# Kernel optimization log

Measured on AMD Instinct MI355X. Metric: run time of the kernel, lower is better.

Reference implementation:

```python
import jax, jax.numpy as jnp
import numpy as np

N = 1024
DIM = 128
HEADS = 8
DK = DIM // HEADS
EDIM = 16
EPS = 1e-5
NEG = -10000.0


def _lin(k, din, dout):
    return jax.random.normal(k, (din, dout), jnp.float32) * (1.0 / np.sqrt(din))


def setup_inputs() -> dict:
    key = jax.random.key(0)
    ks = jax.random.split(key, 10)
    mask = jax.random.randint(ks[2], (N, N), 0, 2).astype(bool)
    mask = mask | jnp.eye(N, dtype=bool)  # self-loops always valid
    return {
        "x": jax.random.normal(ks[0], (N, DIM), jnp.float32),
        "edge_feat": jax.random.normal(ks[1], (N, N, EDIM), jnp.float32),
        "mask": mask,
        "Wq": _lin(ks[3], DIM, DIM), "bq": jnp.zeros((DIM,), jnp.float32),
        "Wk": _lin(ks[4], DIM, DIM), "bk": jnp.zeros((DIM,), jnp.float32),
        "Wv": _lin(ks[5], DIM, DIM), "bv": jnp.zeros((DIM,), jnp.float32),
        "Wae": _lin(ks[6], EDIM, HEADS), "bae": jnp.zeros((HEADS,), jnp.float32),
        "Wve": _lin(ks[7], EDIM, DIM), "bve": jnp.zeros((DIM,), jnp.float32),
        "Wo": _lin(ks[8], DIM, DIM), "bo": jnp.zeros((DIM,), jnp.float32),
        "gamma": jnp.ones((DIM,), jnp.float32),
        "beta": jnp.zeros((DIM,), jnp.float32),
    }


def reference(x, edge_feat, mask, Wq, bq, Wk, bk, Wv, bv, Wae, bae, Wve, bve, Wo, bo, gamma, beta):
    n, dim = x.shape
    heads = bae.shape[0]
    dk = dim // heads
    # pre-LayerNorm
    mu = jnp.mean(x, axis=-1, keepdims=True)
    var = jnp.mean(jnp.square(x - mu), axis=-1, keepdims=True)
    h = (x - mu) * jax.lax.rsqrt(var + EPS) * gamma + beta
    q = (h @ Wq + bq).reshape(n, heads, dk)
    k = (h @ Wk + bk).reshape(n, heads, dk)
    v = (h @ Wv + bv).reshape(n, heads, dk)
    # attention logits with per-edge additive bias: (n, m, heads)
    att = jnp.einsum('nhd,mhd->nmh', q, k) / np.sqrt(dk).astype(np.float32)
    att = att + edge_feat @ Wae + bae
    att = jnp.where(mask[..., None], att, NEG)
    alpha = jax.nn.softmax(att, axis=1)  # softmax over source nodes m
    # edge-conditioned values: msg_{nm} = v_m + U(e_{nm})
    edge_val = (edge_feat @ Wve + bve).reshape(n, n, heads, dk)
    out = jnp.einsum('nmh,mhd->nhd', alpha, v) + jnp.einsum('nmh,nmhd->nhd', alpha, edge_val)
    out = out.reshape(n, dim) @ Wo + bo
    return x + out
```

## Files before the change

### kernel.cpp

```cpp
#include <hip/hip_runtime.h>
#include <hip/hip_bf16.h>

#define NNODE 1024
#define DIM 128
#define HEADS 8
#define DK 16
#define EDIM 16
#define BN 8
#define MR 32
#define EF_ROW 20
#define EF_NSTR 644
#define LOG2E 1.44269504f

__global__ __launch_bounds__(384)
void ln_qkv_kernel(const float* __restrict__ x,
                   const float* __restrict__ Wq, const float* __restrict__ bq,
                   const float* __restrict__ Wk, const float* __restrict__ bk,
                   const float* __restrict__ Wv, const float* __restrict__ bv,
                   const float* __restrict__ gamma, const float* __restrict__ beta,
                   float* __restrict__ qg, float* __restrict__ kg, float* __restrict__ vg) {
    const int n = blockIdx.x;
    const int t = threadIdx.x;
    __shared__ float hrow[DIM];
    __shared__ float part[4];

    float xv = 0.f;
    if (t < 128) {
        xv = x[n * DIM + t];
        float v = xv;
        #pragma unroll
        for (int off = 32; off >= 1; off >>= 1) v += __shfl_xor(v, off);
        if ((t & 63) == 0) part[t >> 6] = v;
    }
    __syncthreads();
    const float mu = (part[0] + part[1]) * (1.0f / DIM);
    const float dx = xv - mu;
    if (t < 128) {
        float v = dx * dx;
        #pragma unroll
        for (int off = 32; off >= 1; off >>= 1) v += __shfl_xor(v, off);
        if ((t & 63) == 0) part[2 + (t >> 6)] = v;
    }
    __syncthreads();
    if (t < 128) {
        const float var = (part[2] + part[3]) * (1.0f / DIM);
        hrow[t] = dx * rsqrtf(var + 1e-5f) * gamma[t] + beta[t];
    }
    __syncthreads();

    const int which = t >> 7;
    const int col = t & 127;
    const float* W = (which == 0) ? Wq : (which == 1) ? Wk : Wv;
    const float* b = (which == 0) ? bq : (which == 1) ? bk : bv;
    float* o       = (which == 0) ? qg : (which == 1) ? kg : vg;
    float acc = b[col];
    #pragma unroll 16
    for (int i = 0; i < DIM; ++i) acc = fmaf(hrow[i], W[i * DIM + col], acc);
    o[n * DIM + col] = acc;
}

__global__ __launch_bounds__(256, 2)
void attn_kernel(const float* __restrict__ qg, const float* __restrict__ kg,
                 const float* __restrict__ vg, const float* __restrict__ ef,
                 const int* __restrict__ mask,
                 const float* __restrict__ Wae, const float* __restrict__ bae,
                 float* __restrict__ acc) {
    const int t = threadIdx.x;
    const int s  = t >> 5;
    const int np = (t >> 3) & 3;
    const int h  = t & 7;
    const int wid = t >> 6, lane = t & 63;
    const int bx = blockIdx.x;
    const int n0 = (bx >> 5) * BN;
    const int mb = (bx & 31) * MR;

    __shared__ float ef_lds[BN * EF_NSTR];
    __shared__ int   mk_lds[BN * 34];

    #pragma unroll
    for (int r = 0; r < 4; ++r) {
        const int idx = t + 256 * r;
        const int nn = idx >> 7;
        const int mm = (idx >> 2) & 31;
        const int q4 = idx & 3;
        const float4 ev = *(const float4*)(ef + ((size_t)(n0 + nn) * NNODE + mb + mm) * EDIM + q4 * 4);
        *(float4*)&ef_lds[nn * EF_NSTR + mm * EF_ROW + q4 * 4] = ev;
    }
    {
        const int nn = t >> 5, mm = t & 31;
        mk_lds[nn * 34 + mm] = mask[(size_t)(n0 + nn) * NNODE + (mb + mm)];
    }
    float qreg[2][DK];
    #pragma unroll
    for (int hf = 0; hf < 2; ++hf) {
        const float* qp = qg + (size_t)(n0 + np + 4 * hf) * DIM + h * DK;
        #pragma unroll
        for (int d4 = 0; d4 < 4; ++d4) {
            const float4 qv = *(const float4*)(qp + d4 * 4);
            qreg[hf][d4 * 4 + 0] = qv.x; qreg[hf][d4 * 4 + 1] = qv.y;
            qreg[hf][d4 * 4 + 2] = qv.z; qreg[hf][d4 * 4 + 3] = qv.w;
        }
    }
    float waec[EDIM];
    #pragma unroll
    for (int e = 0; e < EDIM; ++e) waec[e] = Wae[e * HEADS + h] * LOG2E;
    const float baeh = bae[h] * LOG2E;

    float sl[2] = {0.f, 0.f};
    float accv[2][DK], accT[2][EDIM];
    #pragma unroll
    for (int hf = 0; hf < 2; ++hf) {
        #pragma unroll
        for (int d = 0; d < DK; ++d) accv[hf][d] = 0.f;
        #pragma unroll
        for (int e = 0; e < EDIM; ++e) accT[hf][e] = 0.f;
    }

    __syncthreads();

    #pragma unroll 1
    for (int j = 0; j < 4; ++j) {
        const int m = j * 8 + s;
        const size_t gm = (size_t)(mb + m);
        float kk[DK], vv[DK];
        const float* kp = kg + gm * DIM + h * DK;
        const float* vp = vg + gm * DIM + h * DK;
        #pragma unroll
        for (int d4 = 0; d4 < 4; ++d4) {
            const float4 k4 = *(const float4*)(kp + d4 * 4);
            kk[d4 * 4 + 0] = k4.x; kk[d4 * 4 + 1] = k4.y;
            kk[d4 * 4 + 2] = k4.z; kk[d4 * 4 + 3] = k4.w;
            const float4 v4 = *(const float4*)(vp + d4 * 4);
            vv[d4 * 4 + 0] = v4.x; vv[d4 * 4 + 1] = v4.y;
            vv[d4 * 4 + 2] = v4.z; vv[d4 * 4 + 3] = v4.w;
        }
        #pragma unroll
        for (int hf = 0; hf < 2; ++hf) {
            const int n = np + 4 * hf;
            const float* ep = &ef_lds[n * EF_NSTR + m * EF_ROW];
            float efv[EDIM];
            #pragma unroll
            for (int e4 = 0; e4 < 4; ++e4) {
                const float4 ev = *(const float4*)(ep + e4 * 4);
                efv[e4 * 4 + 0] = ev.x; efv[e4 * 4 + 1] = ev.y;
                efv[e4 * 4 + 2] = ev.z; efv[e4 * 4 + 3] = ev.w;
            }
            float bias = baeh, dot = 0.f;
            #pragma unroll
            for (int e = 0; e < EDIM; ++e) bias = fmaf(efv[e], waec[e], bias);
            #pragma unroll
            for (int d = 0; d < DK; ++d) dot = fmaf(qreg[hf][d], kk[d], dot);
            const float lg = fmaf(dot, 0.25f * LOG2E, bias);
            const float p = mk_lds[n * 34 + m] ? __builtin_amdgcn_exp2f(lg) : 0.f;
            sl[hf] += p;
            #pragma unroll
            for (int d = 0; d < DK; ++d) accv[hf][d] = fmaf(p, vv[d], accv[hf][d]);
            #pragma unroll
            for (int e = 0; e < EDIM; ++e) accT[hf][e] = fmaf(p, efv[e], accT[hf][e]);
        }
    }

    #pragma unroll
    for (int hf = 0; hf < 2; ++hf) {
        sl[hf] += __shfl_xor(sl[hf], 32);
        #pragma unroll
        for (int d = 0; d < DK; ++d) accv[hf][d] += __shfl_xor(accv[hf][d], 32);
        #pragma unroll
        for (int e = 0; e < EDIM; ++e) accT[hf][e] += __shfl_xor(accT[hf][e], 32);
    }
    __syncthreads();
    float* redA = ef_lds;
    float* redB = ef_lds + BN * HEADS * 33;
    if (lane < 32 && wid < 2) {
        float* base = (wid == 0) ? redA : redB;
        #pragma unroll
        for (int hf = 0; hf < 2; ++hf) {
            float* rp = base + ((np + 4 * hf) * 8 + h) * 33;
            rp[0] = sl[hf];
            #pragma unroll
            for (int d = 0; d < DK; ++d) rp[1 + d] = accv[hf][d];
            #pragma unroll
            for (int e = 0; e < EDIM; ++e) rp[17 + e] = accT[hf][e];
        }
    }
    __syncthreads();
    if (lane < 32 && wid >= 2) {
        float* base = (wid == 2) ? redA : redB;
        #pragma unroll
        for (int hf = 0; hf < 2; ++hf) {
            float* rp = base + ((np + 4 * hf) * 8 + h) * 33;
            rp[0] += sl[hf];
            #pragma unroll
            for (int d = 0; d < DK; ++d) rp[1 + d] += accv[hf][d];
            #pragma unroll
            for (int e = 0; e < EDIM; ++e) rp[17 + e] += accT[hf][e];
        }
    }
    __syncthreads();
    for (int u = t; u < BN * HEADS * 33; u += 256)
        atomicAdd(&acc[(size_t)n0 * HEADS * 33 + u], redA[u] + redB[u]);
}

__global__ __launch_bounds__(128)
void final_kernel(const float* __restrict__ acc,
                  const float* __restrict__ Wve, const float* __restrict__ bve,
                  const float* __restrict__ x,
                  const float* __restrict__ Wo, const float* __restrict__ bo,
                  float* __restrict__ out) {
    const int n = blockIdx.x, t = threadIdx.x;
    __shared__ float ab[HEADS * 33];
    __shared__ float orow[DIM];
    for (int u = t; u < HEADS * 33; u += 128) ab[u] = acc[(size_t)n * HEADS * 33 + u];
    __syncthreads();
    const int col = t, hh = col >> 4, dd = col & 15;
    const float slv = ab[hh * 33];
    float acc2 = 0.f;
    #pragma unroll
    for (int e = 0; e < EDIM; ++e) acc2 = fmaf(ab[hh * 33 + 17 + e], Wve[e * DIM + col], acc2);
    orow[col] = (ab[hh * 33 + 1 + dd] + acc2) / slv + bve[col];
    __syncthreads();
    float o = bo[col] + x[(size_t)n * DIM + col];
    #pragma unroll 16
    for (int i = 0; i < DIM; ++i) o = fmaf(orow[i], Wo[i * DIM + col], o);
    out[(size_t)n * DIM + col] = o;
}

extern "C" void kernel_launch(void* const* d_in, const int* in_sizes, int n_in,
                              void* d_out, int out_size, void* d_ws, size_t ws_size,
                              hipStream_t stream) {
    const float* x     = (const float*)d_in[0];
    const float* ef    = (const float*)d_in[1];
    const int*   mask  = (const int*)d_in[2];
    const float* Wq    = (const float*)d_in[3];
    const float* bq    = (const float*)d_in[4];
    const float* Wk    = (const float*)d_in[5];
    const float* bk    = (const float*)d_in[6];
    const float* Wv    = (const float*)d_in[7];
    const float* bv    = (const float*)d_in[8];
    const float* Wae   = (const float*)d_in[9];
    const float* bae   = (const float*)d_in[10];
    const float* Wve   = (const float*)d_in[11];
    const float* bve   = (const float*)d_in[12];
    const float* Wo    = (const float*)d_in[13];
    const float* bo    = (const float*)d_in[14];
    const float* gamma = (const float*)d_in[15];
    const float* beta  = (const float*)d_in[16];

    float* ws = (float*)d_ws;
    float* accb = ws;
    float* qg   = ws + 270336;
    float* kg   = qg + (size_t)NNODE * DIM;
    float* vg   = kg + (size_t)NNODE * DIM;

    hipMemsetAsync(accb, 0, (size_t)NNODE * HEADS * 33 * sizeof(float), stream);
    ln_qkv_kernel<<<NNODE, 384, 0, stream>>>(x, Wq, bq, Wk, bk, Wv, bv, gamma, beta, qg, kg, vg);
    attn_kernel<<<(NNODE / BN) * 32, 256, 0, stream>>>(qg, kg, vg, ef, mask, Wae, bae, accb);
    final_kernel<<<NNODE, 128, 0, stream>>>(accb, Wve, bve, x, Wo, bo, (float*)d_out);
}
```

Measured before the change: 200.4 us.

## Read edge features and mask directly from global, halve m-split block count

Drops the shared-memory staging of edge features and mask, so each thread loads its edge-feature row and mask value straight from global memory inside the loop. The source-node range per block doubles (16 splits instead of 32), so each block loops over 8 iterations with unroll 2 instead of 4, and fewer partial results go through the atomic accumulation. This removes the LDS copy and a barrier but gives up coalesced staging: each thread now reads 64 contiguous bytes per edge with a wider stride between lanes, and there are fewer blocks to hide latency.

```diff
diff --git a/kernel.cpp b/kernel.cpp
--- a/kernel.cpp
+++ b/kernel.cpp
@@ -7,9 +7,9 @@
 #define DK 16
 #define EDIM 16
 #define BN 8
-#define MR 32
-#define EF_ROW 20
-#define EF_NSTR 644
+#define MSPLIT 16
+#define MRANGE (NNODE / MSPLIT)
+#define NJ (MRANGE / 8)
 #define LOG2E 1.44269504f
 
 __global__ __launch_bounds__(384)
@@ -71,25 +71,11 @@
     const int h  = t & 7;
     const int wid = t >> 6, lane = t & 63;
     const int bx = blockIdx.x;
-    const int n0 = (bx >> 5) * BN;
-    const int mb = (bx & 31) * MR;
-
-    __shared__ float ef_lds[BN * EF_NSTR];
-    __shared__ int   mk_lds[BN * 34];
-
-    #pragma unroll
-    for (int r = 0; r < 4; ++r) {
-        const int idx = t + 256 * r;
-        const int nn = idx >> 7;
-        const int mm = (idx >> 2) & 31;
-        const int q4 = idx & 3;
-        const float4 ev = *(const float4*)(ef + ((size_t)(n0 + nn) * NNODE + mb + mm) * EDIM + q4 * 4);
-        *(float4*)&ef_lds[nn * EF_NSTR + mm * EF_ROW + q4 * 4] = ev;
-    }
-    {
-        const int nn = t >> 5, mm = t & 31;
-        mk_lds[nn * 34 + mm] = mask[(size_t)(n0 + nn) * NNODE + (mb + mm)];
-    }
+    const int n0 = (bx >> 4) * BN;
+    const int mb = (bx & 15) * MRANGE;
+
+    __shared__ float red2[2 * BN * HEADS * 33];
+
     float qreg[2][DK];
     #pragma unroll
     for (int hf = 0; hf < 2; ++hf) {
@@ -116,15 +102,12 @@
         for (int e = 0; e < EDIM; ++e) accT[hf][e] = 0.f;
     }
 
-    __syncthreads();
-
-    #pragma unroll 1
-    for (int j = 0; j < 4; ++j) {
-        const int m = j * 8 + s;
-        const size_t gm = (size_t)(mb + m);
+    #pragma unroll 2
+    for (int j = 0; j < NJ; ++j) {
+        const int gm = mb + j * 8 + s;
         float kk[DK], vv[DK];
-        const float* kp = kg + gm * DIM + h * DK;
-        const float* vp = vg + gm * DIM + h * DK;
+        const float* kp = kg + (size_t)gm * DIM + h * DK;
+        const float* vp = vg + (size_t)gm * DIM + h * DK;
         #pragma unroll
         for (int d4 = 0; d4 < 4; ++d4) {
             const float4 k4 = *(const float4*)(kp + d4 * 4);
@@ -137,7 +120,7 @@
         #pragma unroll
         for (int hf = 0; hf < 2; ++hf) {
             const int n = np + 4 * hf;
-            const float* ep = &ef_lds[n * EF_NSTR + m * EF_ROW];
+            const float* ep = ef + ((size_t)(n0 + n) * NNODE + gm) * EDIM;
             float efv[EDIM];
             #pragma unroll
             for (int e4 = 0; e4 < 4; ++e4) {
@@ -145,13 +128,14 @@
                 efv[e4 * 4 + 0] = ev.x; efv[e4 * 4 + 1] = ev.y;
                 efv[e4 * 4 + 2] = ev.z; efv[e4 * 4 + 3] = ev.w;
             }
+            const int mk = mask[(size_t)(n0 + n) * NNODE + gm];
             float bias = baeh, dot = 0.f;
             #pragma unroll
             for (int e = 0; e < EDIM; ++e) bias = fmaf(efv[e], waec[e], bias);
             #pragma unroll
             for (int d = 0; d < DK; ++d) dot = fmaf(qreg[hf][d], kk[d], dot);
             const float lg = fmaf(dot, 0.25f * LOG2E, bias);
-            const float p = mk_lds[n * 34 + m] ? __builtin_amdgcn_exp2f(lg) : 0.f;
+            const float p = mk ? __builtin_amdgcn_exp2f(lg) : 0.f;
             sl[hf] += p;
             #pragma unroll
             for (int d = 0; d < DK; ++d) accv[hf][d] = fmaf(p, vv[d], accv[hf][d]);
@@ -168,9 +152,8 @@
         #pragma unroll
         for (int e = 0; e < EDIM; ++e) accT[hf][e] += __shfl_xor(accT[hf][e], 32);
     }
-    __syncthreads();
-    float* redA = ef_lds;
-    float* redB = ef_lds + BN * HEADS * 33;
+    float* redA = red2;
+    float* redB = red2 + BN * HEADS * 33;
     if (lane < 32 && wid < 2) {
         float* base = (wid == 0) ? redA : redB;
         #pragma unroll
@@ -254,6 +237,6 @@
 
     hipMemsetAsync(accb, 0, (size_t)NNODE * HEADS * 33 * sizeof(float), stream);
     ln_qkv_kernel<<<NNODE, 384, 0, stream>>>(x, Wq, bq, Wk, bk, Wv, bv, gamma, beta, qg, kg, vg);
-    attn_kernel<<<(NNODE / BN) * 32, 256, 0, stream>>>(qg, kg, vg, ef, mask, Wae, bae, accb);
+    attn_kernel<<<(NNODE / BN) * MSPLIT, 256, 0, stream>>>(qg, kg, vg, ef, mask, Wae, bae, accb);
     final_kernel<<<NNODE, 128, 0, stream>>>(accb, Wve, bve, x, Wo, bo, (float*)d_out);
 }
```

New measurement: 191.1 us. 1.05x faster.
